# Performance work log

Hardware: AMD Instinct MI355X
Metric: run time of the kernel (lower is better)

Reference implementation:

```python
import jax, jax.numpy as jnp
import numpy as np

N = 10000        # nodes
E = 320000       # edges (avg degree 32)
W = 256          # width (assert width >= 256)
H = 8            # num_head (RESCALE_EDGE assumed (1,1) -> nhead=8, dhead=32)
D = W // H       # per-head dim
BOND = 33        # EMBED_BOND[0]
BAG = 3          # indices per edge bag
EPS_GN = 1e-5


def setup_inputs() -> dict:
    key = jax.random.key(0)
    ks = jax.random.split(key, 12)
    x = jax.random.normal(ks[0], (N, W), dtype=jnp.float32)
    edge_idx = jax.random.randint(ks[1], (2, E), 0, N)
    edge_attr = jax.random.randint(ks[2], (E, BAG), 0, BOND)
    # node in-degree wrt scatter target edge_idx[1], clamped to >= 1
    deg = jax.ops.segment_sum(jnp.ones((E,), jnp.float32), edge_idx[1], num_segments=N)
    deg = jnp.maximum(deg, 1.0)
    s = 1.0 / np.sqrt(W)
    W_src = jax.random.normal(ks[3], (W, W), dtype=jnp.float32) * s
    W_tgt = jax.random.normal(ks[4], (W, W), dtype=jnp.float32) * s
    emb = jax.random.normal(ks[5], (BOND, W), dtype=jnp.float32) * 0.02
    emb = emb.at[0].set(0.0)  # padding_idx=0 row is zeros
    sd = 1.0 / np.sqrt(D)
    W_gate = jax.random.normal(ks[6], (H, D, D), dtype=jnp.float32) * sd  # grouped conv1d k=1
    W_val = jax.random.normal(ks[7], (H, D, D), dtype=jnp.float32) * sd
    W_post = jax.random.normal(ks[8], (W, W), dtype=jnp.float32) * s
    deg_param = jnp.zeros((W,), jnp.float32) - 0.01  # DegreeLayer degree_init
    return {"x": x, "deg": deg, "edge_idx": edge_idx, "edge_attr": edge_attr,
            "W_src": W_src, "W_tgt": W_tgt, "emb": emb,
            "W_gate": W_gate, "W_val": W_val, "W_post": W_post,
            "deg_param": deg_param}


def reference(x, deg, edge_idx, edge_attr, W_src, W_tgt, emb, W_gate, W_val, W_post, deg_param):
    # src/tgt 1x1 Conv1d == per-node linear, then edge gather
    xs = x @ W_src.T                      # [N, W]
    xt = x @ W_tgt.T                      # [N, W]
    xx = xs[edge_idx[0]] + xt[edge_idx[1]]  # [E, W]

    # EmbeddingBag(mode='mean', padding_idx=0): padded entries excluded
    mask = (edge_attr != 0).astype(xx.dtype)            # [E, BAG]
    bag = jnp.einsum('ebc,eb->ec', emb[edge_attr], mask)  # [E, W]
    cnt = jnp.maximum(mask.sum(-1, keepdims=True), 1.0)
    gate_bias = bag / cnt

    # GroupNorm(H, W, affine=False) over [E, W, 1]
    xg = xx.reshape(-1, H, D)
    mu = xg.mean(-1, keepdims=True)
    var = xg.var(-1, keepdims=True)
    xn = (xg - mu) / jnp.sqrt(var + EPS_GN)              # [E, H, D]

    # gated grouped 1x1 convs (dropout is identity at eval)
    gin = xn + gate_bias.reshape(-1, H, D)
    gate = jax.nn.relu(jnp.einsum('ehd,hfd->ehf', gin, W_gate))
    val = jnp.einsum('ehd,hfd->ehf', xn, W_val)
    act = (gate * val).reshape(-1, W)                    # [E, W]
    out_e = act @ W_post.T                               # [E, W]

    # scatter-sum to nodes, then degree rescale
    agg = jax.ops.segment_sum(out_e, edge_idx[1], num_segments=x.shape[0])
    return jnp.power(deg[:, None], deg_param) * agg      # [N, W]
```

## Files before the change

### kernel.cpp

```cpp
#include <hip/hip_runtime.h>

#define WID 256
#define EPS_GN 1e-5f

typedef __bf16 v8bf __attribute__((ext_vector_type(8)));
typedef __bf16 v2bf __attribute__((ext_vector_type(2)));
typedef float  v4f  __attribute__((ext_vector_type(4)));

__device__ inline unsigned short f2b(float f) {
    unsigned int u = __builtin_bit_cast(unsigned int, f);
    unsigned int r = (u + 0x7fffu + ((u >> 16) & 1u)) >> 16;
    return (unsigned short)r;
}
__device__ inline __bf16 f2bf(float f) {
    unsigned short s = f2b(f);
    return __builtin_bit_cast(__bf16, s);
}
__device__ inline float lo16(unsigned int u) { return __builtin_bit_cast(float, u << 16); }
__device__ inline float hi16(unsigned int u) { return __builtin_bit_cast(float, u & 0xffff0000u); }

#if __has_builtin(__builtin_amdgcn_cvt_pk_bf16_f32)
__device__ inline unsigned int pkbf(float a, float b) {
    v2bf r = __builtin_amdgcn_cvt_pk_bf16_f32(a, b);
    return __builtin_bit_cast(unsigned int, r);
}
#else
__device__ inline unsigned int pkbf(float a, float b) {
    return (unsigned int)f2b(a) | ((unsigned int)f2b(b) << 16);
}
#endif

#if __has_builtin(__builtin_amdgcn_fdot2_f32_bf16)
__device__ inline float pairsum(unsigned int u, float s) {
    v2bf p = __builtin_bit_cast(v2bf, u);
    v2bf ones = __builtin_bit_cast(v2bf, 0x3f803f80u);
    return __builtin_amdgcn_fdot2_f32_bf16(p, ones, s, false);
}
#else
__device__ inline float pairsum(unsigned int u, float s) {
    return s + lo16(u) + hi16(u);
}
#endif

__device__ inline v8bf ld_w8(const float* __restrict__ p) {
    float4 a = *(const float4*)p, b = *(const float4*)(p + 4);
    unsigned int u0 = pkbf(a.x, a.y), u1 = pkbf(a.z, a.w);
    unsigned int u2 = pkbf(b.x, b.y), u3 = pkbf(b.z, b.w);
    uint4 pk = make_uint4(u0, u1, u2, u3);
    return __builtin_bit_cast(v8bf, pk);
}

__global__ __launch_bounds__(256, 2)
void prepproj_k(const float* __restrict__ x, const float* __restrict__ Wsrc,
                const float* __restrict__ Wtgt, const float* __restrict__ Wp,
                const float* __restrict__ Wg, const float* __restrict__ Wv,
                const float* __restrict__ emb, const int* __restrict__ eidx,
                unsigned short* __restrict__ xsb, unsigned short* __restrict__ xtb,
                unsigned short* __restrict__ Wpb, unsigned short* __restrict__ Wgb,
                unsigned short* __restrict__ Wvb, unsigned short* __restrict__ embWgT,
                int* __restrict__ cnt, float* __restrict__ aggact,
                int N, int E, int BOND, int PB, int AUX) {
    __shared__ unsigned short ab[32 * 264];
    int t = threadIdx.x, b = blockIdx.x;

    if (b >= PB) {
        int atid = (b - PB) * 256 + t, asz = AUX * 256;
        for (int i = atid; i < 65536; i += asz) Wpb[i] = f2b(Wp[i]);
        for (int i = atid; i < 8192; i += asz) { Wgb[i] = f2b(Wg[i]); Wvb[i] = f2b(Wv[i]); }
        for (int i = atid; i < 16384; i += asz) {
            int j = i >> 6, k = i & 63;
            float sacc = 0.f;
            if (k < BOND) {
                int h = j >> 5, f = j & 31;
                const float* er = emb + (size_t)k * WID + h * 32;
                const float* wr = Wg + h * 1024 + f * 32;
#pragma unroll
                for (int d = 0; d < 32; d++) sacc += er[d] * wr[d];
            }
            embWgT[j * 64 + k] = f2b(sacc);
        }
        {
            float4* ap = (float4*)aggact;
            int n4 = (N * WID) >> 2;
            for (int i = atid; i < n4; i += asz) ap[i] = make_float4(0.f, 0.f, 0.f, 0.f);
        }
        for (int i = atid; i < E; i += asz) atomicAdd(&cnt[eidx[E + i]], 1);
        return;
    }

    int n0 = b * 32;
#pragma unroll
    for (int ch = 0; ch < 8; ch++) {
        int flat = ch * 1024 + t * 4;
        int row = flat >> 8, col = flat & 255;
        int n = n0 + row;
        float4 v = (n < N) ? *(const float4*)&x[(size_t)n * WID + col]
                           : make_float4(0.f, 0.f, 0.f, 0.f);
        *(uint2*)&ab[row * 264 + col] = make_uint2(pkbf(v.x, v.y), pkbf(v.z, v.w));
    }
    __syncthreads();
    int w = t >> 6, lane = t & 63, m = lane & 15, kg = lane >> 4;
#pragma unroll
    for (int pass = 0; pass < 2; pass++) {
        const float* Wf = pass ? Wtgt : Wsrc;
        unsigned short* outp = pass ? xtb : xsb;
        v4f acc[2][4];
#pragma unroll
        for (int mt = 0; mt < 2; mt++)
#pragma unroll
            for (int nt = 0; nt < 4; nt++) acc[mt][nt] = (v4f){0.f, 0.f, 0.f, 0.f};
#pragma unroll
        for (int kt = 0; kt < 8; kt++) {
            int k0 = kt * 32 + kg * 8;
            v8bf a0 = *(const v8bf*)&ab[m * 264 + k0];
            v8bf a1 = *(const v8bf*)&ab[(16 + m) * 264 + k0];
#pragma unroll
            for (int nt = 0; nt < 4; nt++) {
                int j = w * 64 + nt * 16 + m;
                v8bf bfr = ld_w8(&Wf[j * 256 + k0]);
                acc[0][nt] = __builtin_amdgcn_mfma_f32_16x16x32_bf16(a0, bfr, acc[0][nt], 0, 0, 0);
                acc[1][nt] = __builtin_amdgcn_mfma_f32_16x16x32_bf16(a1, bfr, acc[1][nt], 0, 0, 0);
            }
        }
#pragma unroll
        for (int mt = 0; mt < 2; mt++)
#pragma unroll
            for (int r = 0; r < 4; r++) {
                int n = n0 + mt * 16 + kg * 4 + r;
                if (n < N)
#pragma unroll
                    for (int nt = 0; nt < 4; nt++)
                        outp[(size_t)n * WID + w * 64 + nt * 16 + m] = f2b(acc[mt][nt][r]);
            }
    }
}

__global__ void scan_k(const int* __restrict__ cnt, int* __restrict__ cur, int N) {
    __shared__ int part[1024];
    int t = threadIdx.x;
    int C = (N + 1023) / 1024;
    int s = 0;
    for (int i = 0; i < C; i++) { int idx = t * C + i; if (idx < N) s += cnt[idx]; }
    part[t] = s;
    __syncthreads();
    for (int d = 1; d < 1024; d <<= 1) {
        int v = (t >= d) ? part[t - d] : 0;
        __syncthreads();
        part[t] += v;
        __syncthreads();
    }
    int base = (t == 0) ? 0 : part[t - 1];
    for (int i = 0; i < C; i++) {
        int idx = t * C + i;
        if (idx < N) { cur[idx] = base; base += cnt[idx]; }
    }
}

__global__ void scat_k(const int* __restrict__ eidx, int* __restrict__ cur,
                       int* __restrict__ perm, int E) {
    int i = blockIdx.x * 256 + threadIdx.x;
    if (i < E) { int p = atomicAdd(&cur[eidx[E + i]], 1); perm[p] = i; }
}

__global__ __launch_bounds__(256, 7)
void edge_k(const unsigned short* __restrict__ xsb, const unsigned short* __restrict__ xtb,
            const int* __restrict__ eidx, const int* __restrict__ eattr,
            const int* __restrict__ perm, const unsigned short* __restrict__ Wgb,
            const unsigned short* __restrict__ Wvb, const unsigned short* __restrict__ embWgT,
            float* __restrict__ aggact, int E, int NT, int PER) {
    __shared__ unsigned short xxb[8704];
    __shared__ unsigned short Mld[32 * 72];
    __shared__ int src_s[32], tgt_s[32];
    __shared__ int segmask_s;

    int tile = (blockIdx.x & 7) * PER + (blockIdx.x >> 3);
    if (tile >= NT) return;
    int t = threadIdx.x;
    int e0 = tile * 32;
    int ne = min(32, E - e0);

    {
        int tgtv = -1;
        if (t < 32) {
            int p = (t < ne) ? perm[e0 + t] : -1;
            src_s[t] = (p >= 0) ? eidx[p] : 0;
            tgtv = (p >= 0) ? eidx[E + p] : -1;
            tgt_s[t] = (tgtv >= 0) ? tgtv : 0;
            int a0 = 0, a1 = 0, a2 = 0;
            if (p >= 0) {
                const int* ap = eattr + (size_t)p * 3;
                a0 = ap[0]; a1 = ap[1]; a2 = ap[2];
            }
            unsigned int* Mr = (unsigned int*)&Mld[t * 72];
#pragma unroll
            for (int q = 0; q < 32; q++) Mr[q] = 0;
            int c = (a0 != 0) + (a1 != 0) + (a2 != 0);
            float inv = (p >= 0 && c > 0) ? 1.f / (float)c : 0.f;
            float wa = inv * (float)(1 + (a1 == a0) + (a2 == a0));
            float wb = inv * (float)(1 + (a2 == a1));
            Mld[t * 72 + a0] = f2b(wa);
            if (a1 != a0) Mld[t * 72 + a1] = f2b(wb);
            if (a2 != a0 && a2 != a1) Mld[t * 72 + a2] = f2b(inv);
        }
        if (t < 64) {
            int nxt = __shfl_down(tgtv, 1);
            bool flag = (t < ne) && ((t == ne - 1) || (nxt != tgtv));
            unsigned long long bal = __ballot(flag);
            if (t == 0) segmask_s = (int)(unsigned int)bal;
        }
    }
    __syncthreads();

    {
        int e = t >> 3, c = t & 7;
        int sn = src_s[e], g = tgt_s[e];
        bool live = (e < ne);
        const uint4* ps = (const uint4*)(xsb + (size_t)sn * WID);
        const uint4* pt = (const uint4*)(xtb + (size_t)g * WID);
        uint4 us[4], ut[4];
#pragma unroll
        for (int i = 0; i < 4; i++) { us[i] = ps[c + 8 * i]; ut[i] = pt[c + 8 * i]; }
        float v[4][8], sum[4], sq[4];
#pragma unroll
        for (int i = 0; i < 4; i++) {
            const unsigned int* au = (const unsigned int*)&us[i];
            const unsigned int* bu = (const unsigned int*)&ut[i];
            sum[i] = 0.f; sq[i] = 0.f;
#pragma unroll
            for (int q = 0; q < 4; q++) {
                float x0 = lo16(au[q]) + lo16(bu[q]);
                float x1 = hi16(au[q]) + hi16(bu[q]);
                if (!live) { x0 = 0.f; x1 = 0.f; }
                v[i][2 * q] = x0; v[i][2 * q + 1] = x1;
                sum[i] += x0 + x1;
                sq[i] += x0 * x0 + x1 * x1;
            }
        }
#pragma unroll
        for (int mask = 1; mask <= 2; mask <<= 1)
#pragma unroll
            for (int i = 0; i < 4; i++) {
                sum[i] += __shfl_xor(sum[i], mask);
                sq[i]  += __shfl_xor(sq[i], mask);
            }
#pragma unroll
        for (int i = 0; i < 4; i++) {
            float mu = sum[i] * (1.f / 32.f);
            float var = sq[i] * (1.f / 32.f) - mu * mu;
            float rs = rsqrtf(var + EPS_GN);
            float nmr = -mu * rs;
            unsigned int pk[4];
#pragma unroll
            for (int q = 0; q < 4; q++)
                pk[q] = pkbf(fmaf(v[i][2 * q], rs, nmr), fmaf(v[i][2 * q + 1], rs, nmr));
            *(uint4*)&xxb[e * 264 + (c + 8 * i) * 8] = make_uint4(pk[0], pk[1], pk[2], pk[3]);
        }
    }
    __syncthreads();

    {
        int w = t >> 6, lane = t & 63, m = lane & 15, kg = lane >> 4;
        v8bf axn[2][2], aM[2][2];
#pragma unroll
        for (int mt = 0; mt < 2; mt++) {
            int row = mt * 16 + m;
            axn[0][mt] = *(const v8bf*)&xxb[row * 264 + (w * 2 + 0) * 32 + kg * 8];
            axn[1][mt] = *(const v8bf*)&xxb[row * 264 + (w * 2 + 1) * 32 + kg * 8];
            aM[mt][0] = *(const v8bf*)&Mld[row * 72 + kg * 8];
            aM[mt][1] = *(const v8bf*)&Mld[row * 72 + 32 + kg * 8];
        }
        __syncthreads();
        v4f z = {0.f, 0.f, 0.f, 0.f};
#pragma unroll
        for (int hh = 0; hh < 2; hh++) {
            int h = w * 2 + hh;
#pragma unroll
            for (int nt = 0; nt < 2; nt++) {
                int fj = nt * 16 + m;
                int j = h * 32 + fj;
                v8bf bWg = *(const v8bf*)&Wgb[h * 1024 + fj * 32 + kg * 8];
                v8bf bWv = *(const v8bf*)&Wvb[h * 1024 + fj * 32 + kg * 8];
                v8bf bE0 = *(const v8bf*)&embWgT[j * 64 + kg * 8];
                v8bf bE1 = *(const v8bf*)&embWgT[j * 64 + 32 + kg * 8];
#pragma unroll
                for (int mt = 0; mt < 2; mt++) {
                    v4f cgm = __builtin_amdgcn_mfma_f32_16x16x32_bf16(axn[hh][mt], bWg, z, 0, 0, 0);
                    cgm = __builtin_amdgcn_mfma_f32_16x16x32_bf16(aM[mt][0], bE0, cgm, 0, 0, 0);
                    cgm = __builtin_amdgcn_mfma_f32_16x16x32_bf16(aM[mt][1], bE1, cgm, 0, 0, 0);
                    v4f cv = __builtin_amdgcn_mfma_f32_16x16x32_bf16(axn[hh][mt], bWv, z, 0, 0, 0);
                    float a0 = fmaxf(cgm[0], 0.f) * cv[0];
                    float a1 = fmaxf(cgm[1], 0.f) * cv[1];
                    float a2 = fmaxf(cgm[2], 0.f) * cv[2];
                    float a3 = fmaxf(cgm[3], 0.f) * cv[3];
                    int e0i = mt * 16 + kg * 4;
                    *(unsigned int*)&xxb[j * 34 + e0i]     = pkbf(a0, a1);
                    *(unsigned int*)&xxb[j * 34 + e0i + 2] = pkbf(a2, a3);
                }
            }
        }
    }
    __syncthreads();

    {
        unsigned int mask = (unsigned int)__builtin_amdgcn_readfirstlane(segmask_s);
        float sum = 0.f;
#pragma unroll
        for (int i = 0; i < 16; i++) {
            unsigned int r = *(const unsigned int*)&xxb[t * 34 + 2 * i];
            if (!((mask >> (2 * i)) & 1)) {
                sum = pairsum(r, sum);
                if ((mask >> (2 * i + 1)) & 1) {
                    int tg = __builtin_amdgcn_readfirstlane(tgt_s[2 * i + 1]);
                    atomicAdd(&aggact[(size_t)tg * WID + t], sum);
                    sum = 0.f;
                }
            } else {
                sum += lo16(r);
                int tg = __builtin_amdgcn_readfirstlane(tgt_s[2 * i]);
                atomicAdd(&aggact[(size_t)tg * WID + t], sum);
                sum = hi16(r);
                if ((mask >> (2 * i + 1)) & 1) {
                    int tg2 = __builtin_amdgcn_readfirstlane(tgt_s[2 * i + 1]);
                    atomicAdd(&aggact[(size_t)tg2 * WID + t], sum);
                    sum = 0.f;
                }
            }
        }
    }
}

__global__ __launch_bounds__(256, 2)
void post_k(const float* __restrict__ aggact, const unsigned short* __restrict__ Wpb,
            const float* __restrict__ deg, const float* __restrict__ dp,
            float* __restrict__ out, int N) {
    __shared__ unsigned short ab[32 * 264];
    __shared__ float degl[32];
    int t = threadIdx.x;
    int n0 = blockIdx.x * 32;
#pragma unroll
    for (int ch = 0; ch < 8; ch++) {
        int flat = ch * 1024 + t * 4;
        int row = flat >> 8, col = flat & 255;
        int n = n0 + row;
        float4 v = (n < N) ? *(const float4*)&aggact[(size_t)n * WID + col]
                           : make_float4(0.f, 0.f, 0.f, 0.f);
        *(uint2*)&ab[row * 264 + col] = make_uint2(pkbf(v.x, v.y), pkbf(v.z, v.w));
    }
    if (t < 32) {
        int n = n0 + t;
        degl[t] = (n < N) ? log2f(deg[n]) : 0.f;
    }
    __syncthreads();
    int w = t >> 6, lane = t & 63, m = lane & 15, kg = lane >> 4;
    v4f acc[2][4];
#pragma unroll
    for (int mt = 0; mt < 2; mt++)
#pragma unroll
        for (int nt = 0; nt < 4; nt++) acc[mt][nt] = (v4f){0.f, 0.f, 0.f, 0.f};
#pragma unroll
    for (int kt = 0; kt < 8; kt++) {
        int k0 = kt * 32 + kg * 8;
        v8bf a0 = *(const v8bf*)&ab[m * 264 + k0];
        v8bf a1 = *(const v8bf*)&ab[(16 + m) * 264 + k0];
#pragma unroll
        for (int nt = 0; nt < 4; nt++) {
            int j = w * 64 + nt * 16 + m;
            v8bf b = *(const v8bf*)&Wpb[j * 256 + k0];
            acc[0][nt] = __builtin_amdgcn_mfma_f32_16x16x32_bf16(a0, b, acc[0][nt], 0, 0, 0);
            acc[1][nt] = __builtin_amdgcn_mfma_f32_16x16x32_bf16(a1, b, acc[1][nt], 0, 0, 0);
        }
    }
    float dpv[4];
#pragma unroll
    for (int nt = 0; nt < 4; nt++) dpv[nt] = dp[w * 64 + nt * 16 + m];
#pragma unroll
    for (int mt = 0; mt < 2; mt++)
#pragma unroll
        for (int r = 0; r < 4; r++) {
            int row = mt * 16 + kg * 4 + r;
            int n = n0 + row;
            if (n < N) {
                float ld = degl[row];
#pragma unroll
                for (int nt = 0; nt < 4; nt++)
                    out[(size_t)n * WID + w * 64 + nt * 16 + m] =
                        exp2f(dpv[nt] * ld) * acc[mt][nt][r];
            }
        }
}

extern "C" void kernel_launch(void* const* d_in, const int* in_sizes, int n_in,
                              void* d_out, int out_size, void* d_ws, size_t ws_size,
                              hipStream_t stream) {
    const float* x    = (const float*)d_in[0];
    const float* deg  = (const float*)d_in[1];
    const int*   eidx = (const int*)d_in[2];
    const int*   eatt = (const int*)d_in[3];
    const float* Wsrc = (const float*)d_in[4];
    const float* Wtgt = (const float*)d_in[5];
    const float* emb  = (const float*)d_in[6];
    const float* Wg   = (const float*)d_in[7];
    const float* Wv   = (const float*)d_in[8];
    const float* Wp   = (const float*)d_in[9];
    const float* dp   = (const float*)d_in[10];
    int N = in_sizes[0] / WID;
    int E = in_sizes[2] / 2;
    int BOND = in_sizes[6] / WID;

    float* ws     = (float*)d_ws;
    float* aggact = ws;
    int*   cnt    = (int*)(aggact + (size_t)N * WID);
    int*   cur    = cnt + N;
    int*   perm   = cur + N;
    unsigned short* xsb = (unsigned short*)(perm + E);
    unsigned short* xtb = xsb + (size_t)N * WID;
    unsigned short* Wpb = xtb + (size_t)N * WID;
    unsigned short* Wgb = Wpb + 65536;
    unsigned short* Wvb = Wgb + 8192;
    unsigned short* embWgT = Wvb + 8192;

    int PB = (N + 31) / 32;
    int AUX = 128;
    int NT = (E + 31) / 32;
    int PER = (NT + 7) / 8;

    hipMemsetAsync(cnt, 0, (size_t)N * sizeof(int), stream);
    prepproj_k<<<PB + AUX, 256, 0, stream>>>(x, Wsrc, Wtgt, Wp, Wg, Wv, emb, eidx,
                                             xsb, xtb, Wpb, Wgb, Wvb, embWgT, cnt, aggact,
                                             N, E, BOND, PB, AUX);
    scan_k<<<1, 1024, 0, stream>>>(cnt, cur, N);
    scat_k<<<(E + 255) / 256, 256, 0, stream>>>(eidx, cur, perm, E);
    edge_k<<<PER * 8, 256, 0, stream>>>(xsb, xtb, eidx, eatt, perm, Wgb, Wvb, embWgT,
                                        aggact, E, NT, PER);
    post_k<<<(N + 31) / 32, 256, 0, stream>>>(aggact, Wpb, deg, dp, (float*)d_out, N);
}
```

Measured before the change: 235.9 us.

## Load GroupNorm inputs directly into MFMA fragments, skip LDS staging

The edge kernel now gathers source and target rows straight into the MFMA A-operand register layout and computes the per-head GroupNorm statistics with cross-lane shuffles. This removes the LDS round-trip of normalized features and two block barriers, and shrinks shared memory to just the activation buffer. The scan kernel also stages the degree counts in LDS so global memory is read once and written coalesced. Occupancy hint drops from 7 to 6 waves to leave room for the extra registers.

```diff
diff --git a/kernel.cpp b/kernel.cpp
--- a/kernel.cpp
+++ b/kernel.cpp
@@ -136,11 +136,16 @@
 }
 
 __global__ void scan_k(const int* __restrict__ cnt, int* __restrict__ cur, int N) {
+    __shared__ int buf[10240];
     __shared__ int part[1024];
     int t = threadIdx.x;
-    int C = (N + 1023) / 1024;
+    int C = (N + 1023) >> 10;
+    int M = C << 10;
+    for (int i = t; i < M; i += 1024) buf[i] = (i < N) ? cnt[i] : 0;
+    __syncthreads();
+    int base0 = t * C;
     int s = 0;
-    for (int i = 0; i < C; i++) { int idx = t * C + i; if (idx < N) s += cnt[idx]; }
+    for (int i = 0; i < C; i++) s += buf[base0 + i];
     part[t] = s;
     __syncthreads();
     for (int d = 1; d < 1024; d <<= 1) {
@@ -151,9 +156,13 @@
     }
     int base = (t == 0) ? 0 : part[t - 1];
     for (int i = 0; i < C; i++) {
-        int idx = t * C + i;
-        if (idx < N) { cur[idx] = base; base += cnt[idx]; }
-    }
+        int idx = base0 + i;
+        int v = buf[idx];
+        buf[idx] = base;
+        base += v;
+    }
+    __syncthreads();
+    for (int i = t; i < N; i += 1024) cur[i] = buf[i];
 }
 
 __global__ void scat_k(const int* __restrict__ eidx, int* __restrict__ cur,
@@ -162,13 +171,13 @@
     if (i < E) { int p = atomicAdd(&cur[eidx[E + i]], 1); perm[p] = i; }
 }
 
-__global__ __launch_bounds__(256, 7)
+__global__ __launch_bounds__(256, 6)
 void edge_k(const unsigned short* __restrict__ xsb, const unsigned short* __restrict__ xtb,
             const int* __restrict__ eidx, const int* __restrict__ eattr,
             const int* __restrict__ perm, const unsigned short* __restrict__ Wgb,
             const unsigned short* __restrict__ Wvb, const unsigned short* __restrict__ embWgT,
             float* __restrict__ aggact, int E, int NT, int PER) {
-    __shared__ unsigned short xxb[8704];
+    __shared__ unsigned short actb[256 * 34];
     __shared__ unsigned short Mld[32 * 72];
     __shared__ int src_s[32], tgt_s[32];
     __shared__ int segmask_s;
@@ -211,65 +220,56 @@
     }
     __syncthreads();
 
-    {
-        int e = t >> 3, c = t & 7;
-        int sn = src_s[e], g = tgt_s[e];
+    int w = t >> 6, lane = t & 63, m = lane & 15, kg = lane >> 4;
+
+    v8bf axn[2][2];
+#pragma unroll
+    for (int mt = 0; mt < 2; mt++) {
+        int e = mt * 16 + m;
         bool live = (e < ne);
-        const uint4* ps = (const uint4*)(xsb + (size_t)sn * WID);
-        const uint4* pt = (const uint4*)(xtb + (size_t)g * WID);
-        uint4 us[4], ut[4];
-#pragma unroll
-        for (int i = 0; i < 4; i++) { us[i] = ps[c + 8 * i]; ut[i] = pt[c + 8 * i]; }
-        float v[4][8], sum[4], sq[4];
-#pragma unroll
-        for (int i = 0; i < 4; i++) {
-            const unsigned int* au = (const unsigned int*)&us[i];
-            const unsigned int* bu = (const unsigned int*)&ut[i];
-            sum[i] = 0.f; sq[i] = 0.f;
-#pragma unroll
-            for (int q = 0; q < 4; q++) {
-                float x0 = lo16(au[q]) + lo16(bu[q]);
-                float x1 = hi16(au[q]) + hi16(bu[q]);
+        const unsigned short* prs = xsb + (size_t)src_s[e] * WID;
+        const unsigned short* prt = xtb + (size_t)tgt_s[e] * WID;
+#pragma unroll
+        for (int hh = 0; hh < 2; hh++) {
+            int col = (w * 2 + hh) * 32 + kg * 8;
+            uint4 us = *(const uint4*)(prs + col);
+            uint4 ut = *(const uint4*)(prt + col);
+            const unsigned int* au = (const unsigned int*)&us;
+            const unsigned int* bu = (const unsigned int*)&ut;
+            float v[8];
+            float s = 0.f, q = 0.f;
+#pragma unroll
+            for (int qq = 0; qq < 4; qq++) {
+                float x0 = lo16(au[qq]) + lo16(bu[qq]);
+                float x1 = hi16(au[qq]) + hi16(bu[qq]);
                 if (!live) { x0 = 0.f; x1 = 0.f; }
-                v[i][2 * q] = x0; v[i][2 * q + 1] = x1;
-                sum[i] += x0 + x1;
-                sq[i] += x0 * x0 + x1 * x1;
-            }
-        }
-#pragma unroll
-        for (int mask = 1; mask <= 2; mask <<= 1)
-#pragma unroll
-            for (int i = 0; i < 4; i++) {
-                sum[i] += __shfl_xor(sum[i], mask);
-                sq[i]  += __shfl_xor(sq[i], mask);
-            }
-#pragma unroll
-        for (int i = 0; i < 4; i++) {
-            float mu = sum[i] * (1.f / 32.f);
-            float var = sq[i] * (1.f / 32.f) - mu * mu;
+                v[2 * qq] = x0; v[2 * qq + 1] = x1;
+                s += x0 + x1;
+                q += x0 * x0 + x1 * x1;
+            }
+            s += __shfl_xor(s, 16); q += __shfl_xor(q, 16);
+            s += __shfl_xor(s, 32); q += __shfl_xor(q, 32);
+            float mu = s * (1.f / 32.f);
+            float var = q * (1.f / 32.f) - mu * mu;
             float rs = rsqrtf(var + EPS_GN);
             float nmr = -mu * rs;
-            unsigned int pk[4];
-#pragma unroll
-            for (int q = 0; q < 4; q++)
-                pk[q] = pkbf(fmaf(v[i][2 * q], rs, nmr), fmaf(v[i][2 * q + 1], rs, nmr));
-            *(uint4*)&xxb[e * 264 + (c + 8 * i) * 8] = make_uint4(pk[0], pk[1], pk[2], pk[3]);
-        }
-    }
-    __syncthreads();
+            uint4 pk = make_uint4(
+                pkbf(fmaf(v[0], rs, nmr), fmaf(v[1], rs, nmr)),
+                pkbf(fmaf(v[2], rs, nmr), fmaf(v[3], rs, nmr)),
+                pkbf(fmaf(v[4], rs, nmr), fmaf(v[5], rs, nmr)),
+                pkbf(fmaf(v[6], rs, nmr), fmaf(v[7], rs, nmr)));
+            axn[hh][mt] = __builtin_bit_cast(v8bf, pk);
+        }
+    }
 
     {
-        int w = t >> 6, lane = t & 63, m = lane & 15, kg = lane >> 4;
-        v8bf axn[2][2], aM[2][2];
+        v8bf aM[2][2];
 #pragma unroll
         for (int mt = 0; mt < 2; mt++) {
             int row = mt * 16 + m;
-            axn[0][mt] = *(const v8bf*)&xxb[row * 264 + (w * 2 + 0) * 32 + kg * 8];
-            axn[1][mt] = *(const v8bf*)&xxb[row * 264 + (w * 2 + 1) * 32 + kg * 8];
             aM[mt][0] = *(const v8bf*)&Mld[row * 72 + kg * 8];
             aM[mt][1] = *(const v8bf*)&Mld[row * 72 + 32 + kg * 8];
         }
-        __syncthreads();
         v4f z = {0.f, 0.f, 0.f, 0.f};
 #pragma unroll
         for (int hh = 0; hh < 2; hh++) {
@@ -293,8 +293,8 @@
                     float a2 = fmaxf(cgm[2], 0.f) * cv[2];
                     float a3 = fmaxf(cgm[3], 0.f) * cv[3];
                     int e0i = mt * 16 + kg * 4;
-                    *(unsigned int*)&xxb[j * 34 + e0i]     = pkbf(a0, a1);
-                    *(unsigned int*)&xxb[j * 34 + e0i + 2] = pkbf(a2, a3);
+                    *(unsigned int*)&actb[j * 34 + e0i]     = pkbf(a0, a1);
+                    *(unsigned int*)&actb[j * 34 + e0i + 2] = pkbf(a2, a3);
                 }
             }
         }
@@ -306,7 +306,7 @@
         float sum = 0.f;
 #pragma unroll
         for (int i = 0; i < 16; i++) {
-            unsigned int r = *(const unsigned int*)&xxb[t * 34 + 2 * i];
+            unsigned int r = *(const unsigned int*)&actb[t * 34 + 2 * i];
             if (!((mask >> (2 * i)) & 1)) {
                 sum = pairsum(r, sum);
                 if ((mask >> (2 * i + 1)) & 1) {
```

Measured after the change: 246.5 us. +4.5%, slower.

## Pre-cast projection weights to bf16 in separate kernel and stage scan in LDS

Applied to the files above, without the earlier changes.

Adds a cast kernel that converts W_src/W_tgt (and the other weights) to bf16 once, and zeroes the count array in place of a memset. The projection GEMM then loads bf16 weights directly instead of re-reading fp32 and packing per block. The scan kernel stages counts in shared memory so that global reads and writes are coalesced rather than strided per thread. The cost is one extra kernel launch and a serial dependency before the projection.

```diff
diff --git a/kernel.cpp b/kernel.cpp
--- a/kernel.cpp
+++ b/kernel.cpp
@@ -11,10 +11,6 @@
     unsigned int u = __builtin_bit_cast(unsigned int, f);
     unsigned int r = (u + 0x7fffu + ((u >> 16) & 1u)) >> 16;
     return (unsigned short)r;
-}
-__device__ inline __bf16 f2bf(float f) {
-    unsigned short s = f2b(f);
-    return __builtin_bit_cast(__bf16, s);
 }
 __device__ inline float lo16(unsigned int u) { return __builtin_bit_cast(float, u << 16); }
 __device__ inline float hi16(unsigned int u) { return __builtin_bit_cast(float, u & 0xffff0000u); }
@@ -42,43 +38,45 @@
 }
 #endif
 
-__device__ inline v8bf ld_w8(const float* __restrict__ p) {
-    float4 a = *(const float4*)p, b = *(const float4*)(p + 4);
-    unsigned int u0 = pkbf(a.x, a.y), u1 = pkbf(a.z, a.w);
-    unsigned int u2 = pkbf(b.x, b.y), u3 = pkbf(b.z, b.w);
-    uint4 pk = make_uint4(u0, u1, u2, u3);
-    return __builtin_bit_cast(v8bf, pk);
+__global__ void cast_k(const float* __restrict__ Wsrc, const float* __restrict__ Wtgt,
+                       const float* __restrict__ Wp, const float* __restrict__ Wg,
+                       const float* __restrict__ Wv, const float* __restrict__ emb,
+                       unsigned short* __restrict__ Wsb, unsigned short* __restrict__ Wtb,
+                       unsigned short* __restrict__ Wpb, unsigned short* __restrict__ Wgb,
+                       unsigned short* __restrict__ Wvb, unsigned short* __restrict__ embWgT,
+                       int* __restrict__ cnt, int N, int BOND) {
+    int i = blockIdx.x * 256 + threadIdx.x;
+    int gsz = gridDim.x * 256;
+    for (int j = i; j < N; j += gsz) cnt[j] = 0;
+    for (int j = i; j < 65536; j += gsz) {
+        Wsb[j] = f2b(Wsrc[j]); Wtb[j] = f2b(Wtgt[j]); Wpb[j] = f2b(Wp[j]);
+    }
+    for (int j = i; j < 8192; j += gsz) { Wgb[j] = f2b(Wg[j]); Wvb[j] = f2b(Wv[j]); }
+    for (int j = i; j < 16384; j += gsz) {
+        int jr = j >> 6, k = j & 63;
+        float sacc = 0.f;
+        if (k < BOND) {
+            int h = jr >> 5, f = jr & 31;
+            const float* er = emb + (size_t)k * WID + h * 32;
+            const float* wr = Wg + h * 1024 + f * 32;
+#pragma unroll
+            for (int d = 0; d < 32; d++) sacc += er[d] * wr[d];
+        }
+        embWgT[jr * 64 + k] = f2b(sacc);
+    }
 }
 
 __global__ __launch_bounds__(256, 2)
-void prepproj_k(const float* __restrict__ x, const float* __restrict__ Wsrc,
-                const float* __restrict__ Wtgt, const float* __restrict__ Wp,
-                const float* __restrict__ Wg, const float* __restrict__ Wv,
-                const float* __restrict__ emb, const int* __restrict__ eidx,
+void prepproj_k(const float* __restrict__ x, const unsigned short* __restrict__ Wsb,
+                const unsigned short* __restrict__ Wtb, const int* __restrict__ eidx,
                 unsigned short* __restrict__ xsb, unsigned short* __restrict__ xtb,
-                unsigned short* __restrict__ Wpb, unsigned short* __restrict__ Wgb,
-                unsigned short* __restrict__ Wvb, unsigned short* __restrict__ embWgT,
                 int* __restrict__ cnt, float* __restrict__ aggact,
-                int N, int E, int BOND, int PB, int AUX) {
+                int N, int E, int PB, int AUX) {
     __shared__ unsigned short ab[32 * 264];
     int t = threadIdx.x, b = blockIdx.x;
 
     if (b >= PB) {
         int atid = (b - PB) * 256 + t, asz = AUX * 256;
-        for (int i = atid; i < 65536; i += asz) Wpb[i] = f2b(Wp[i]);
-        for (int i = atid; i < 8192; i += asz) { Wgb[i] = f2b(Wg[i]); Wvb[i] = f2b(Wv[i]); }
-        for (int i = atid; i < 16384; i += asz) {
-            int j = i >> 6, k = i & 63;
-            float sacc = 0.f;
-            if (k < BOND) {
-                int h = j >> 5, f = j & 31;
-                const float* er = emb + (size_t)k * WID + h * 32;
-                const float* wr = Wg + h * 1024 + f * 32;
-#pragma unroll
-                for (int d = 0; d < 32; d++) sacc += er[d] * wr[d];
-            }
-            embWgT[j * 64 + k] = f2b(sacc);
-        }
         {
             float4* ap = (float4*)aggact;
             int n4 = (N * WID) >> 2;
@@ -102,7 +100,7 @@
     int w = t >> 6, lane = t & 63, m = lane & 15, kg = lane >> 4;
 #pragma unroll
     for (int pass = 0; pass < 2; pass++) {
-        const float* Wf = pass ? Wtgt : Wsrc;
+        const unsigned short* Wb = pass ? Wtb : Wsb;
         unsigned short* outp = pass ? xtb : xsb;
         v4f acc[2][4];
 #pragma unroll
@@ -117,7 +115,7 @@
 #pragma unroll
             for (int nt = 0; nt < 4; nt++) {
                 int j = w * 64 + nt * 16 + m;
-                v8bf bfr = ld_w8(&Wf[j * 256 + k0]);
+                v8bf bfr = *(const v8bf*)&Wb[j * 256 + k0];
                 acc[0][nt] = __builtin_amdgcn_mfma_f32_16x16x32_bf16(a0, bfr, acc[0][nt], 0, 0, 0);
                 acc[1][nt] = __builtin_amdgcn_mfma_f32_16x16x32_bf16(a1, bfr, acc[1][nt], 0, 0, 0);
             }
@@ -136,11 +134,16 @@
 }
 
 __global__ void scan_k(const int* __restrict__ cnt, int* __restrict__ cur, int N) {
+    __shared__ int buf[10240];
     __shared__ int part[1024];
     int t = threadIdx.x;
-    int C = (N + 1023) / 1024;
+    int C = (N + 1023) >> 10;
+    int M = C << 10;
+    for (int i = t; i < M; i += 1024) buf[i] = (i < N) ? cnt[i] : 0;
+    __syncthreads();
+    int base0 = t * C;
     int s = 0;
-    for (int i = 0; i < C; i++) { int idx = t * C + i; if (idx < N) s += cnt[idx]; }
+    for (int i = 0; i < C; i++) s += buf[base0 + i];
     part[t] = s;
     __syncthreads();
     for (int d = 1; d < 1024; d <<= 1) {
@@ -151,9 +154,13 @@
     }
     int base = (t == 0) ? 0 : part[t - 1];
     for (int i = 0; i < C; i++) {
-        int idx = t * C + i;
-        if (idx < N) { cur[idx] = base; base += cnt[idx]; }
-    }
+        int idx = base0 + i;
+        int v = buf[idx];
+        buf[idx] = base;
+        base += v;
+    }
+    __syncthreads();
+    for (int i = t; i < N; i += 1024) cur[i] = buf[i];
 }
 
 __global__ void scat_k(const int* __restrict__ eidx, int* __restrict__ cur,
@@ -414,7 +421,9 @@
     int*   perm   = cur + N;
     unsigned short* xsb = (unsigned short*)(perm + E);
     unsigned short* xtb = xsb + (size_t)N * WID;
-    unsigned short* Wpb = xtb + (size_t)N * WID;
+    unsigned short* Wsb = xtb + (size_t)N * WID;
+    unsigned short* Wtb = Wsb + 65536;
+    unsigned short* Wpb = Wtb + 65536;
     unsigned short* Wgb = Wpb + 65536;
     unsigned short* Wvb = Wgb + 8192;
     unsigned short* embWgT = Wvb + 8192;
@@ -424,10 +433,10 @@
     int NT = (E + 31) / 32;
     int PER = (NT + 7) / 8;
 
-    hipMemsetAsync(cnt, 0, (size_t)N * sizeof(int), stream);
-    prepproj_k<<<PB + AUX, 256, 0, stream>>>(x, Wsrc, Wtgt, Wp, Wg, Wv, emb, eidx,
-                                             xsb, xtb, Wpb, Wgb, Wvb, embWgT, cnt, aggact,
-                                             N, E, BOND, PB, AUX);
+    cast_k<<<320, 256, 0, stream>>>(Wsrc, Wtgt, Wp, Wg, Wv, emb,
+                                    Wsb, Wtb, Wpb, Wgb, Wvb, embWgT, cnt, N, BOND);
+    prepproj_k<<<PB + AUX, 256, 0, stream>>>(x, Wsb, Wtb, eidx, xsb, xtb, cnt, aggact,
+                                             N, E, PB, AUX);
     scan_k<<<1, 1024, 0, stream>>>(cnt, cur, N);
     scat_k<<<(E + 255) / 256, 256, 0, stream>>>(eidx, cur, perm, E);
     edge_k<<<PER * 8, 256, 0, stream>>>(xsb, xtb, eidx, eatt, perm, Wgb, Wvb, embWgT,
```

Measured after the change: 231.4 us. About the same (-1.9%).
